# Performance work log

Hardware: AMD Instinct MI355X
Metric: run time of the kernel (lower is better)

## Reference

```python
import jax, jax.numpy as jnp
import numpy as np

INPUT_DIM, HIDDEN_DIM, OUTPUT_DIM = 256, 64, 64
N_NODES, N_EDGES = 100000, 1200000


def setup_inputs() -> dict:
    key = jax.random.key(0)
    k1, k2, k3, k4 = jax.random.split(key, 4)
    x = jax.random.normal(k1, (N_NODES, INPUT_DIM), dtype=jnp.float32)
    edge_index = jax.random.randint(k2, (2, N_EDGES), 0, N_NODES, dtype=jnp.int64)
    # torch Linear weight layout: [out_features, in_features], xavier_uniform init
    def xavier(k, shape):
        fan_out, fan_in = shape
        lim = float(np.sqrt(6.0 / (fan_in + fan_out)))
        return jax.random.uniform(k, shape, minval=-lim, maxval=lim, dtype=jnp.float32)
    W1 = xavier(k3, (HIDDEN_DIM, INPUT_DIM))
    b1 = jnp.zeros((HIDDEN_DIM,), dtype=jnp.float32)
    W2 = xavier(k4, (OUTPUT_DIM, HIDDEN_DIM))
    b2 = jnp.zeros((OUTPUT_DIM,), dtype=jnp.float32)
    return {"x": x, "edge_index": edge_index, "W1": W1, "b1": b1, "W2": W2, "b2": b2}


def reference(x, edge_index, W1, b1, W2, b2):
    N = x.shape[0]
    loops = jnp.arange(N, dtype=edge_index.dtype)
    # GCNConv default: add self-loops, symmetric deg^-1/2 normalization
    src = jnp.concatenate([edge_index[0], loops])  # message sources (x_j)
    dst = jnp.concatenate([edge_index[1], loops])  # aggregation targets
    deg = jax.ops.segment_sum(jnp.ones_like(src, dtype=x.dtype), dst, num_segments=N)
    dinv = jnp.where(deg > 0, jax.lax.rsqrt(jnp.maximum(deg, 1e-12)), 0.0)
    norm = dinv[src] * dinv[dst]  # [E+N]

    def gcn_layer(h, W, b):
        h = h @ W.T                      # dense linear transform [N, out]
        msg = h[src] * norm[:, None]     # gather + scale [E+N, out]
        agg = jax.ops.segment_sum(msg, dst, num_segments=N)  # scatter-add
        return agg + b

    h = jax.nn.relu(gcn_layer(x, W1, b1))
    out = jax.nn.relu(gcn_layer(h, W2, b2))
    return out
```

## Files before the change

### kernel.cpp

```cpp
#include <hip/hip_runtime.h>

static constexpr int NN  = 100000;
static constexpr int NE  = 1200000;
static constexpr int KIN = 256;
static constexpr int HID = 64;

static constexpr int BSH   = 7;
static constexpr int NPB   = 1 << BSH;
static constexpr int NB    = (NN + NPB - 1) / NPB;
static constexpr int CAP   = 4096;
static constexpr int CHUNK = 8192;
static constexpr int NBK   = (NE + CHUNK - 1) / CHUNK;

typedef __attribute__((ext_vector_type(8))) __bf16 bf16v8;
typedef __attribute__((ext_vector_type(4))) float f32x4;

__device__ __forceinline__ float bf2f(unsigned short u) {
  return __uint_as_float(((unsigned int)u) << 16);
}
__device__ __forceinline__ unsigned short f2bf(float f) {
  unsigned int b = __float_as_uint(f);
  return (unsigned short)((b + 0x7FFFu + ((b >> 16) & 1u)) >> 16);
}

__global__ void k_wconv2z(const float* __restrict__ W1, __bf16* __restrict__ Whi1, __bf16* __restrict__ Wlo1,
                          const float* __restrict__ W2, __bf16* __restrict__ Whi2, __bf16* __restrict__ Wlo2,
                          int* __restrict__ gcur) {
  int i = blockIdx.x * 256 + threadIdx.x;
  constexpr int n1 = HID * KIN;
  if (i < n1) {
    float v = W1[i];
    __bf16 h = (__bf16)v;
    Whi1[i] = h;
    Wlo1[i] = (__bf16)(v - (float)h);
  } else if (i < n1 + HID * HID) {
    int j = i - n1;
    float v = W2[j];
    __bf16 h = (__bf16)v;
    Whi2[j] = h;
    Wlo2[j] = (__bf16)(v - (float)h);
  }
  if (i < NB) gcur[i] = 0;
}

__global__ void __launch_bounds__(256) k_bin1p(const int* __restrict__ ed, int* __restrict__ gcur,
                                               unsigned* __restrict__ binned) {
  __shared__ int lcnt[NB];
  __shared__ int lbase[NB];
  int t = threadIdx.x, blk = blockIdx.x;
  for (int i = t; i < NB; i += 256) lcnt[i] = 0;
  __syncthreads();
  int base = blk * CHUNK;
  #pragma unroll
  for (int it = 0; it < CHUNK / 256; ++it) {
    int e = base + it * 256 + t;
    if (e < NE) atomicAdd(&lcnt[ed[NE + e] >> BSH], 1);
  }
  __syncthreads();
  for (int i = t; i < NB; i += 256) {
    int c = lcnt[i];
    lbase[i] = (c > 0) ? atomicAdd(&gcur[i], c) : 0;
    lcnt[i] = 0;
  }
  __syncthreads();
  #pragma unroll
  for (int it = 0; it < CHUNK / 256; ++it) {
    int e = base + it * 256 + t;
    if (e < NE) {
      int src = ed[e];
      int dst = ed[NE + e];
      int b = dst >> BSH;
      int r = atomicAdd(&lcnt[b], 1);
      binned[(size_t)b * CAP + lbase[b] + r] = (unsigned)src | ((unsigned)(dst & (NPB - 1)) << 17);
    }
  }
}

__global__ void __launch_bounds__(256) k_degcsr(const unsigned* __restrict__ binned,
                                                const int* __restrict__ gcur,
                                                int* __restrict__ deg, float* __restrict__ dinv,
                                                int* __restrict__ rp, int* __restrict__ csr) {
  __shared__ int d[NPB];
  __shared__ int sc[NPB];
  __shared__ int cur[NPB];
  int t = threadIdx.x, b = blockIdx.x;
  if (t < NPB) { d[t] = 0; cur[t] = 0; }
  __syncthreads();
  const int n = gcur[b];
  const unsigned* win = binned + (size_t)b * CAP;
  for (int i = t; i < n; i += 256) atomicAdd(&d[win[i] >> 17], 1);
  __syncthreads();
  if (t < NPB) sc[t] = d[t];
  __syncthreads();
  #pragma unroll
  for (int off = 1; off < NPB; off <<= 1) {
    int x = (t < NPB && t >= off) ? sc[t - off] : 0;
    __syncthreads();
    if (t < NPB) sc[t] += x;
    __syncthreads();
  }
  if (t < NPB) {
    int node = b * NPB + t;
    if (node < NN) {
      deg[node] = d[t];
      dinv[node] = rsqrtf((float)(d[t] + 1));
      rp[node] = b * CAP + sc[t] - d[t];
    }
  }
  __syncthreads();
  for (int i = t; i < n; i += 256) {
    unsigned u = win[i];
    int src = (int)(u & 0x1FFFFu);
    int dl  = (int)(u >> 17);
    int r = atomicAdd(&cur[dl], 1);
    csr[(size_t)b * CAP + (sc[dl] - d[dl]) + r] = src;
  }
}

template<int K, int MODE>
__global__ void __launch_bounds__(256, 4)
k_gemm(const float* __restrict__ X, const __bf16* __restrict__ Whi, const __bf16* __restrict__ Wlo,
       const float* __restrict__ dinv, const float* __restrict__ bias, void* __restrict__ Yv) {
  constexpr int KT = 32;
  constexpr int NT = K / KT;
  constexpr int LS = 40;
  constexpr int CS = 68;
  __shared__ __align__(16) char smem[4 * 64 * LS * 2];
  __bf16* xh = (__bf16*)smem;
  __bf16* xl = xh + 64 * LS;
  __bf16* wh = xl + 64 * LS;
  __bf16* wl = wh + 64 * LS;
  float*  cl = (float*)smem;

  const int t = threadIdx.x;
  const int l = t & 63;
  const int wc = (t >> 6) * 16;
  const int rowbase = blockIdx.x * 64;

  f32x4 acc[4];
  #pragma unroll
  for (int rt = 0; rt < 4; ++rt) acc[rt] = (f32x4){0.f, 0.f, 0.f, 0.f};

  const int sr = t >> 2;
  const int kc = (t & 3) * 8;

  for (int kt = 0; kt < NT; ++kt) {
    __syncthreads();
    {
      int gr = rowbase + sr;
      float4 v0 = make_float4(0.f, 0.f, 0.f, 0.f), v1 = v0;
      if (gr < NN) {
        const float* xp = X + (size_t)gr * K + kt * KT + kc;
        v0 = *reinterpret_cast<const float4*>(xp);
        v1 = *reinterpret_cast<const float4*>(xp + 4);
      }
      float e[8] = {v0.x, v0.y, v0.z, v0.w, v1.x, v1.y, v1.z, v1.w};
      bf16v8 hv, lv;
      #pragma unroll
      for (int j = 0; j < 8; ++j) {
        __bf16 h = (__bf16)e[j];
        hv[j] = h;
        lv[j] = (__bf16)(e[j] - (float)h);
      }
      *reinterpret_cast<bf16v8*>(&xh[sr * LS + kc]) = hv;
      *reinterpret_cast<bf16v8*>(&xl[sr * LS + kc]) = lv;
      *reinterpret_cast<bf16v8*>(&wh[sr * LS + kc]) =
          *reinterpret_cast<const bf16v8*>(Whi + (size_t)sr * K + kt * KT + kc);
      *reinterpret_cast<bf16v8*>(&wl[sr * LS + kc]) =
          *reinterpret_cast<const bf16v8*>(Wlo + (size_t)sr * K + kt * KT + kc);
    }
    __syncthreads();

    const int bo = (wc + (l & 15)) * LS + (l >> 4) * 8;
    bf16v8 bh = *reinterpret_cast<const bf16v8*>(&wh[bo]);
    bf16v8 bl = *reinterpret_cast<const bf16v8*>(&wl[bo]);
    #pragma unroll
    for (int rt = 0; rt < 4; ++rt) {
      const int ao = (rt * 16 + (l & 15)) * LS + (l >> 4) * 8;
      bf16v8 ah = *reinterpret_cast<const bf16v8*>(&xh[ao]);
      bf16v8 al = *reinterpret_cast<const bf16v8*>(&xl[ao]);
      acc[rt] = __builtin_amdgcn_mfma_f32_16x16x32_bf16(ah, bh, acc[rt], 0, 0, 0);
      acc[rt] = __builtin_amdgcn_mfma_f32_16x16x32_bf16(al, bh, acc[rt], 0, 0, 0);
      acc[rt] = __builtin_amdgcn_mfma_f32_16x16x32_bf16(ah, bl, acc[rt], 0, 0, 0);
    }
  }

  __syncthreads();
  #pragma unroll
  for (int rt = 0; rt < 4; ++rt)
    #pragma unroll
    for (int j = 0; j < 4; ++j)
      cl[(rt * 16 + (l >> 4) * 4 + j) * CS + wc + (l & 15)] = acc[rt][j];
  __syncthreads();

  const int r = t >> 2, cc = (t & 3) * 16;
  const int grow = rowbase + r;
  if (grow < NN) {
    if (MODE == 0) {
      float dv = dinv[grow];
      bf16v8 o0, o1;
      #pragma unroll
      for (int j = 0; j < 8; ++j) o0[j] = (__bf16)(cl[r * CS + cc + j] * dv);
      #pragma unroll
      for (int j = 0; j < 8; ++j) o1[j] = (__bf16)(cl[r * CS + cc + 8 + j] * dv);
      __bf16* yp = (__bf16*)Yv + (size_t)grow * HID + cc;
      *reinterpret_cast<bf16v8*>(yp) = o0;
      *reinterpret_cast<bf16v8*>(yp + 8) = o1;
    } else {
      float* yp = (float*)Yv + (size_t)grow * HID + cc;
      #pragma unroll
      for (int c4 = 0; c4 < 4; ++c4) {
        float4 o;
        o.x = fmaxf(cl[r * CS + cc + c4 * 4 + 0] + bias[cc + c4 * 4 + 0], 0.f);
        o.y = fmaxf(cl[r * CS + cc + c4 * 4 + 1] + bias[cc + c4 * 4 + 1], 0.f);
        o.z = fmaxf(cl[r * CS + cc + c4 * 4 + 2] + bias[cc + c4 * 4 + 2], 0.f);
        o.w = fmaxf(cl[r * CS + cc + c4 * 4 + 3] + bias[cc + c4 * 4 + 3], 0.f);
        *reinterpret_cast<float4*>(yp + c4 * 4) = o;
      }
    }
  }
}

__global__ void __launch_bounds__(256, 8)
k_agg(const unsigned short* __restrict__ T, const int* __restrict__ csr,
      const int* __restrict__ rp, const int* __restrict__ deg,
      const float* __restrict__ dinv, const float* __restrict__ bias,
      unsigned short* __restrict__ Ov) {
  int node = blockIdx.x * 4 + (threadIdx.x >> 6);
  int lane = threadIdx.x & 63;
  float acc = bf2f(T[(size_t)node * HID + lane]);
  int start = rp[node];
  int len = deg[node];
  for (int base = 0; base < len; base += 64) {
    int m = min(64, len - base);
    int idx = (lane < m) ? csr[start + base + lane] : 0;
    for (int c0 = 0; c0 < m; c0 += 16) {
      float part = 0.f;
      #pragma unroll
      for (int i = 0; i < 16; ++i) {
        int e = c0 + i;
        int s = __shfl(idx, e & 63);
        float v = bf2f(T[(size_t)s * HID + lane]);
        part += (e < m) ? v : 0.f;
      }
      acc += part;
    }
  }
  float dv = dinv[node];
  float h = dv * fmaxf(fmaf(dv, acc, bias[lane]), 0.f);
  Ov[(size_t)node * HID + lane] = f2bf(h);
}

__global__ void __launch_bounds__(256, 8)
k_aggemm(const unsigned short* __restrict__ T, const int* __restrict__ csr,
         const int* __restrict__ rp, const int* __restrict__ deg,
         const float* __restrict__ dinv,
         const __bf16* __restrict__ Whi2, const __bf16* __restrict__ Wlo2,
         const float* __restrict__ bias, float* __restrict__ out) {
  constexpr int LS = 72;
  constexpr int CS = 68;
  __shared__ __align__(16) char smem[2 * 64 * LS * 2];
  __bf16* gh = (__bf16*)smem;
  __bf16* gl = gh + 64 * LS;
  float*  cl = (float*)smem;

  const int t = threadIdx.x;
  const int l = t & 63;
  const int w = t >> 6;
  const int rowbase = blockIdx.x * 64;

  for (int i = 0; i < 16; ++i) {
    int node = rowbase + w * 16 + i;
    float gv = 0.f;
    if (node < NN) {
      float acc = bf2f(T[(size_t)node * HID + l]);
      int start = rp[node];
      int len = deg[node];
      for (int base = 0; base < len; base += 64) {
        int m = min(64, len - base);
        int idx = (l < m) ? csr[start + base + l] : 0;
        for (int c0 = 0; c0 < m; c0 += 16) {
          float part = 0.f;
          #pragma unroll
          for (int j = 0; j < 16; ++j) {
            int e = c0 + j;
            int s = __shfl(idx, e & 63);
            float v = bf2f(T[(size_t)s * HID + l]);
            part += (e < m) ? v : 0.f;
          }
          acc += part;
        }
      }
      gv = dinv[node] * acc;
    }
    __bf16 h = (__bf16)gv;
    int r = w * 16 + i;
    gh[r * LS + l] = h;
    gl[r * LS + l] = (__bf16)(gv - (float)h);
  }
  __syncthreads();

  const int wc = w * 16;
  f32x4 acc[4];
  #pragma unroll
  for (int rt = 0; rt < 4; ++rt) acc[rt] = (f32x4){0.f, 0.f, 0.f, 0.f};
  #pragma unroll
  for (int kc = 0; kc < 2; ++kc) {
    const size_t wo = (size_t)(wc + (l & 15)) * HID + kc * 32 + (l >> 4) * 8;
    bf16v8 bh = *reinterpret_cast<const bf16v8*>(Whi2 + wo);
    bf16v8 bl = *reinterpret_cast<const bf16v8*>(Wlo2 + wo);
    #pragma unroll
    for (int rt = 0; rt < 4; ++rt) {
      const int ao = (rt * 16 + (l & 15)) * LS + kc * 32 + (l >> 4) * 8;
      bf16v8 ah = *reinterpret_cast<const bf16v8*>(&gh[ao]);
      bf16v8 al = *reinterpret_cast<const bf16v8*>(&gl[ao]);
      acc[rt] = __builtin_amdgcn_mfma_f32_16x16x32_bf16(ah, bh, acc[rt], 0, 0, 0);
      acc[rt] = __builtin_amdgcn_mfma_f32_16x16x32_bf16(al, bh, acc[rt], 0, 0, 0);
      acc[rt] = __builtin_amdgcn_mfma_f32_16x16x32_bf16(ah, bl, acc[rt], 0, 0, 0);
    }
  }
  __syncthreads();
  #pragma unroll
  for (int rt = 0; rt < 4; ++rt)
    #pragma unroll
    for (int j = 0; j < 4; ++j)
      cl[(rt * 16 + (l >> 4) * 4 + j) * CS + wc + (l & 15)] = acc[rt][j];
  __syncthreads();

  const int r = t >> 2, cc = (t & 3) * 16;
  const int grow = rowbase + r;
  if (grow < NN) {
    float* yp = out + (size_t)grow * HID + cc;
    #pragma unroll
    for (int c4 = 0; c4 < 4; ++c4) {
      float4 o;
      o.x = fmaxf(cl[r * CS + cc + c4 * 4 + 0] + bias[cc + c4 * 4 + 0], 0.f);
      o.y = fmaxf(cl[r * CS + cc + c4 * 4 + 1] + bias[cc + c4 * 4 + 1], 0.f);
      o.z = fmaxf(cl[r * CS + cc + c4 * 4 + 2] + bias[cc + c4 * 4 + 2], 0.f);
      o.w = fmaxf(cl[r * CS + cc + c4 * 4 + 3] + bias[cc + c4 * 4 + 3], 0.f);
      *reinterpret_cast<float4*>(yp + c4 * 4) = o;
    }
  }
}

extern "C" void kernel_launch(void* const* d_in, const int* in_sizes, int n_in,
                              void* d_out, int out_size, void* d_ws, size_t ws_size,
                              hipStream_t stream) {
  const float* x  = (const float*)d_in[0];
  const int*   ed = (const int*)d_in[1];
  const float* W1 = (const float*)d_in[2];
  const float* b1 = (const float*)d_in[3];
  const float* W2 = (const float*)d_in[4];
  const float* b2 = (const float*)d_in[5];
  float* out = (float*)d_out;

  char* ws = (char*)d_ws;
  size_t off = 0;
  auto alloc = [&](size_t bytes) {
    char* p = ws + off;
    off = (off + bytes + 255) & ~(size_t)255;
    return p;
  };
  int*      deg    = (int*)alloc((size_t)NN * 4);
  float*    dinv   = (float*)alloc((size_t)NN * 4);
  int*      rp     = (int*)alloc((size_t)NN * 4);
  int*      gcur   = (int*)alloc((size_t)NB * 4);
  unsigned* binned = (unsigned*)alloc((size_t)NB * CAP * 4);
  int*      csr    = (int*)alloc((size_t)NB * CAP * 4);
  unsigned short* T1 = (unsigned short*)alloc((size_t)NN * HID * 2);
  unsigned short* Hp = (unsigned short*)alloc((size_t)NN * HID * 2);
  __bf16*   Whi1   = (__bf16*)alloc((size_t)HID * KIN * 2);
  __bf16*   Wlo1   = (__bf16*)alloc((size_t)HID * KIN * 2);
  __bf16*   Whi2   = (__bf16*)alloc((size_t)HID * HID * 2);
  __bf16*   Wlo2   = (__bf16*)alloc((size_t)HID * HID * 2);

  k_wconv2z<<<(HID * KIN + HID * HID + 255) / 256, 256, 0, stream>>>(W1, Whi1, Wlo1, W2, Whi2, Wlo2, gcur);
  k_bin1p<<<NBK, 256, 0, stream>>>(ed, gcur, binned);
  k_degcsr<<<NB, 256, 0, stream>>>(binned, gcur, deg, dinv, rp, csr);

  const int GB = (NN + 63) / 64;

  k_gemm<KIN, 0><<<GB, 256, 0, stream>>>(x, Whi1, Wlo1, dinv, b1, (void*)T1);
  k_agg<<<NN / 4, 256, 0, stream>>>(T1, csr, rp, deg, dinv, b1, Hp);

  k_aggemm<<<GB, 256, 0, stream>>>(Hp, csr, rp, deg, dinv, Whi2, Wlo2, b2, out);
}
```

Baseline: 154.3 us.

## Prefetch GEMM tiles into registers and interleave two-node gathers in aggregation

The first-layer GEMM now loads the next K tile from global memory into registers while the MFMAs for the current tile run, then writes it to shared memory behind a barrier. This hides global load latency at the cost of extra registers and an extra barrier per iteration. Both aggregation kernels now make each wavefront process two nodes at once, issuing both nodes' 16 gathered loads before reducing them. This raises memory-level parallelism, and launch bounds are lowered from 8 to 6 to leave room for the extra registers, which risks lower occupancy and divergence when the two nodes have different degrees.

Result: slower. 157.9 us (+2.4%).

```diff
diff --git a/kernel.cpp b/kernel.cpp
--- a/kernel.cpp
+++ b/kernel.cpp
@@ -143,33 +143,44 @@
 
   const int sr = t >> 2;
   const int kc = (t & 3) * 8;
+  const int gr = rowbase + sr;
+  const float* xrow = X + (size_t)gr * K + kc;
+
+  float4 pa, pb;
+  bf16v8 pwh, pwl;
+
+  auto loadTile = [&](int kt) {
+    pa = make_float4(0.f, 0.f, 0.f, 0.f);
+    pb = pa;
+    if (gr < NN) {
+      pa = *reinterpret_cast<const float4*>(xrow + kt * KT);
+      pb = *reinterpret_cast<const float4*>(xrow + kt * KT + 4);
+    }
+    size_t wo = (size_t)sr * K + kt * KT + kc;
+    pwh = *reinterpret_cast<const bf16v8*>(Whi + wo);
+    pwl = *reinterpret_cast<const bf16v8*>(Wlo + wo);
+  };
+  auto storeTile = [&]() {
+    float e[8] = {pa.x, pa.y, pa.z, pa.w, pb.x, pb.y, pb.z, pb.w};
+    bf16v8 hv, lv;
+    #pragma unroll
+    for (int j = 0; j < 8; ++j) {
+      __bf16 h = (__bf16)e[j];
+      hv[j] = h;
+      lv[j] = (__bf16)(e[j] - (float)h);
+    }
+    *reinterpret_cast<bf16v8*>(&xh[sr * LS + kc]) = hv;
+    *reinterpret_cast<bf16v8*>(&xl[sr * LS + kc]) = lv;
+    *reinterpret_cast<bf16v8*>(&wh[sr * LS + kc]) = pwh;
+    *reinterpret_cast<bf16v8*>(&wl[sr * LS + kc]) = pwl;
+  };
+
+  loadTile(0);
+  storeTile();
+  __syncthreads();
 
   for (int kt = 0; kt < NT; ++kt) {
-    __syncthreads();
-    {
-      int gr = rowbase + sr;
-      float4 v0 = make_float4(0.f, 0.f, 0.f, 0.f), v1 = v0;
-      if (gr < NN) {
-        const float* xp = X + (size_t)gr * K + kt * KT + kc;
-        v0 = *reinterpret_cast<const float4*>(xp);
-        v1 = *reinterpret_cast<const float4*>(xp + 4);
-      }
-      float e[8] = {v0.x, v0.y, v0.z, v0.w, v1.x, v1.y, v1.z, v1.w};
-      bf16v8 hv, lv;
-      #pragma unroll
-      for (int j = 0; j < 8; ++j) {
-        __bf16 h = (__bf16)e[j];
-        hv[j] = h;
-        lv[j] = (__bf16)(e[j] - (float)h);
-      }
-      *reinterpret_cast<bf16v8*>(&xh[sr * LS + kc]) = hv;
-      *reinterpret_cast<bf16v8*>(&xl[sr * LS + kc]) = lv;
-      *reinterpret_cast<bf16v8*>(&wh[sr * LS + kc]) =
-          *reinterpret_cast<const bf16v8*>(Whi + (size_t)sr * K + kt * KT + kc);
-      *reinterpret_cast<bf16v8*>(&wl[sr * LS + kc]) =
-          *reinterpret_cast<const bf16v8*>(Wlo + (size_t)sr * K + kt * KT + kc);
-    }
-    __syncthreads();
+    if (kt + 1 < NT) loadTile(kt + 1);
 
     const int bo = (wc + (l & 15)) * LS + (l >> 4) * 8;
     bf16v8 bh = *reinterpret_cast<const bf16v8*>(&wh[bo]);
@@ -182,6 +193,12 @@
       acc[rt] = __builtin_amdgcn_mfma_f32_16x16x32_bf16(ah, bh, acc[rt], 0, 0, 0);
       acc[rt] = __builtin_amdgcn_mfma_f32_16x16x32_bf16(al, bh, acc[rt], 0, 0, 0);
       acc[rt] = __builtin_amdgcn_mfma_f32_16x16x32_bf16(ah, bl, acc[rt], 0, 0, 0);
+    }
+
+    if (kt + 1 < NT) {
+      __syncthreads();
+      storeTile();
+      __syncthreads();
     }
   }
 
@@ -221,37 +238,63 @@
   }
 }
 
-__global__ void __launch_bounds__(256, 8)
+__global__ void __launch_bounds__(256, 6)
 k_agg(const unsigned short* __restrict__ T, const int* __restrict__ csr,
       const int* __restrict__ rp, const int* __restrict__ deg,
       const float* __restrict__ dinv, const float* __restrict__ bias,
       unsigned short* __restrict__ Ov) {
-  int node = blockIdx.x * 4 + (threadIdx.x >> 6);
-  int lane = threadIdx.x & 63;
-  float acc = bf2f(T[(size_t)node * HID + lane]);
-  int start = rp[node];
-  int len = deg[node];
-  for (int base = 0; base < len; base += 64) {
-    int m = min(64, len - base);
-    int idx = (lane < m) ? csr[start + base + lane] : 0;
-    for (int c0 = 0; c0 < m; c0 += 16) {
-      float part = 0.f;
-      #pragma unroll
-      for (int i = 0; i < 16; ++i) {
-        int e = c0 + i;
-        int s = __shfl(idx, e & 63);
-        float v = bf2f(T[(size_t)s * HID + lane]);
-        part += (e < m) ? v : 0.f;
-      }
-      acc += part;
-    }
-  }
-  float dv = dinv[node];
-  float h = dv * fmaxf(fmaf(dv, acc, bias[lane]), 0.f);
-  Ov[(size_t)node * HID + lane] = f2bf(h);
-}
-
-__global__ void __launch_bounds__(256, 8)
+  const int lane = threadIdx.x & 63;
+  const int n0 = blockIdx.x * 8 + (threadIdx.x >> 6) * 2;
+  const int n1 = n0 + 1;
+  float acc0 = bf2f(T[(size_t)n0 * HID + lane]);
+  float acc1 = bf2f(T[(size_t)n1 * HID + lane]);
+  const int s0 = rp[n0], l0 = deg[n0];
+  const int s1 = rp[n1], l1 = deg[n1];
+  const int lmax = max(l0, l1);
+  for (int base = 0; base < lmax; base += 64) {
+    const int m0 = min(64, l0 - base);
+    const int m1 = min(64, l1 - base);
+    int idx0 = (lane < m0) ? csr[s0 + base + lane] : 0;
+    int idx1 = (lane < m1) ? csr[s1 + base + lane] : 0;
+    const int cmax = max(m0, m1);
+    for (int c0 = 0; c0 < cmax; c0 += 16) {
+      float v0[16], v1[16];
+      const bool a0 = c0 < m0, a1 = c0 < m1;
+      if (a0) {
+        #pragma unroll
+        for (int i = 0; i < 16; ++i) {
+          int s = __shfl(idx0, (c0 + i) & 63);
+          v0[i] = bf2f(T[(size_t)s * HID + lane]);
+        }
+      }
+      if (a1) {
+        #pragma unroll
+        for (int i = 0; i < 16; ++i) {
+          int s = __shfl(idx1, (c0 + i) & 63);
+          v1[i] = bf2f(T[(size_t)s * HID + lane]);
+        }
+      }
+      if (a0) {
+        float p = 0.f;
+        #pragma unroll
+        for (int i = 0; i < 16; ++i) p += (c0 + i < m0) ? v0[i] : 0.f;
+        acc0 += p;
+      }
+      if (a1) {
+        float p = 0.f;
+        #pragma unroll
+        for (int i = 0; i < 16; ++i) p += (c0 + i < m1) ? v1[i] : 0.f;
+        acc1 += p;
+      }
+    }
+  }
+  float dv0 = dinv[n0];
+  Ov[(size_t)n0 * HID + lane] = f2bf(dv0 * fmaxf(fmaf(dv0, acc0, bias[lane]), 0.f));
+  float dv1 = dinv[n1];
+  Ov[(size_t)n1 * HID + lane] = f2bf(dv1 * fmaxf(fmaf(dv1, acc1, bias[lane]), 0.f));
+}
+
+__global__ void __launch_bounds__(256, 6)
 k_aggemm(const unsigned short* __restrict__ T, const int* __restrict__ csr,
          const int* __restrict__ rp, const int* __restrict__ deg,
          const float* __restrict__ dinv,
@@ -269,34 +312,60 @@
   const int w = t >> 6;
   const int rowbase = blockIdx.x * 64;
 
-  for (int i = 0; i < 16; ++i) {
-    int node = rowbase + w * 16 + i;
-    float gv = 0.f;
-    if (node < NN) {
-      float acc = bf2f(T[(size_t)node * HID + l]);
-      int start = rp[node];
-      int len = deg[node];
-      for (int base = 0; base < len; base += 64) {
-        int m = min(64, len - base);
-        int idx = (l < m) ? csr[start + base + l] : 0;
-        for (int c0 = 0; c0 < m; c0 += 16) {
-          float part = 0.f;
+  for (int i = 0; i < 16; i += 2) {
+    const int n0 = rowbase + w * 16 + i;
+    const int n1 = n0 + 1;
+    const bool va0 = n0 < NN, va1 = n1 < NN;
+    float acc0 = va0 ? bf2f(T[(size_t)n0 * HID + l]) : 0.f;
+    float acc1 = va1 ? bf2f(T[(size_t)n1 * HID + l]) : 0.f;
+    const int s0 = va0 ? rp[n0] : 0, l0 = va0 ? deg[n0] : 0;
+    const int s1 = va1 ? rp[n1] : 0, l1 = va1 ? deg[n1] : 0;
+    const int lmax = max(l0, l1);
+    for (int base = 0; base < lmax; base += 64) {
+      const int m0 = min(64, l0 - base);
+      const int m1 = min(64, l1 - base);
+      int idx0 = (l < m0) ? csr[s0 + base + l] : 0;
+      int idx1 = (l < m1) ? csr[s1 + base + l] : 0;
+      const int cmax = max(m0, m1);
+      for (int c0 = 0; c0 < cmax; c0 += 16) {
+        float v0[16], v1[16];
+        const bool a0 = c0 < m0, a1 = c0 < m1;
+        if (a0) {
           #pragma unroll
           for (int j = 0; j < 16; ++j) {
-            int e = c0 + j;
-            int s = __shfl(idx, e & 63);
-            float v = bf2f(T[(size_t)s * HID + l]);
-            part += (e < m) ? v : 0.f;
+            int s = __shfl(idx0, (c0 + j) & 63);
+            v0[j] = bf2f(T[(size_t)s * HID + l]);
           }
-          acc += part;
-        }
-      }
-      gv = dinv[node] * acc;
-    }
-    __bf16 h = (__bf16)gv;
-    int r = w * 16 + i;
-    gh[r * LS + l] = h;
-    gl[r * LS + l] = (__bf16)(gv - (float)h);
+        }
+        if (a1) {
+          #pragma unroll
+          for (int j = 0; j < 16; ++j) {
+            int s = __shfl(idx1, (c0 + j) & 63);
+            v1[j] = bf2f(T[(size_t)s * HID + l]);
+          }
+        }
+        if (a0) {
+          float p = 0.f;
+          #pragma unroll
+          for (int j = 0; j < 16; ++j) p += (c0 + j < m0) ? v0[j] : 0.f;
+          acc0 += p;
+        }
+        if (a1) {
+          float p = 0.f;
+          #pragma unroll
+          for (int j = 0; j < 16; ++j) p += (c0 + j < m1) ? v1[j] : 0.f;
+          acc1 += p;
+        }
+      }
+    }
+    float g0 = va0 ? dinv[n0] * acc0 : 0.f;
+    float g1 = va1 ? dinv[n1] * acc1 : 0.f;
+    __bf16 h0 = (__bf16)g0, h1 = (__bf16)g1;
+    const int r0 = w * 16 + i;
+    gh[r0 * LS + l] = h0;
+    gl[r0 * LS + l] = (__bf16)(g0 - (float)h0);
+    gh[(r0 + 1) * LS + l] = h1;
+    gl[(r0 + 1) * LS + l] = (__bf16)(g1 - (float)h1);
   }
   __syncthreads();
 
@@ -381,7 +450,7 @@
   const int GB = (NN + 63) / 64;
 
   k_gemm<KIN, 0><<<GB, 256, 0, stream>>>(x, Whi1, Wlo1, dinv, b1, (void*)T1);
-  k_agg<<<NN / 4, 256, 0, stream>>>(T1, csr, rp, deg, dinv, b1, Hp);
+  k_agg<<<NN / 8, 256, 0, stream>>>(T1, csr, rp, deg, dinv, b1, Hp);
 
   k_aggemm<<<GB, 256, 0, stream>>>(Hp, csr, rp, deg, dinv, Whi2, Wlo2, b2, out);
 }
```

## Prefetch GEMM tiles into registers and gather two bf16 features per lane

Applied to the files above, without the earlier changes.

The first-layer GEMM now loads the next K tile from global memory into registers while MFMAs run on the current shared-memory tile, overlapping load latency with compute. Both aggregation kernels now read packed 32-bit words holding two bf16 features. Each half-wave handles alternate edges, so every gather instruction covers two neighbour rows, and the two halves are combined with a lane shuffle. This is meant to cut gather instruction count and raise bytes per load, at the cost of more registers. k_aggemm's launch bounds are lowered from 8 to 6 to allow for that.

After: 145.5 us. 5.7% less time.

```diff
diff --git a/kernel.cpp b/kernel.cpp
--- a/kernel.cpp
+++ b/kernel.cpp
@@ -143,33 +143,44 @@
 
   const int sr = t >> 2;
   const int kc = (t & 3) * 8;
+  const int gr = rowbase + sr;
+  const float* xrow = X + (size_t)gr * K + kc;
+
+  float4 pa, pb;
+  bf16v8 pwh, pwl;
+
+  auto loadTile = [&](int kt) {
+    pa = make_float4(0.f, 0.f, 0.f, 0.f);
+    pb = pa;
+    if (gr < NN) {
+      pa = *reinterpret_cast<const float4*>(xrow + kt * KT);
+      pb = *reinterpret_cast<const float4*>(xrow + kt * KT + 4);
+    }
+    size_t wo = (size_t)sr * K + kt * KT + kc;
+    pwh = *reinterpret_cast<const bf16v8*>(Whi + wo);
+    pwl = *reinterpret_cast<const bf16v8*>(Wlo + wo);
+  };
+  auto storeTile = [&]() {
+    float e[8] = {pa.x, pa.y, pa.z, pa.w, pb.x, pb.y, pb.z, pb.w};
+    bf16v8 hv, lv;
+    #pragma unroll
+    for (int j = 0; j < 8; ++j) {
+      __bf16 h = (__bf16)e[j];
+      hv[j] = h;
+      lv[j] = (__bf16)(e[j] - (float)h);
+    }
+    *reinterpret_cast<bf16v8*>(&xh[sr * LS + kc]) = hv;
+    *reinterpret_cast<bf16v8*>(&xl[sr * LS + kc]) = lv;
+    *reinterpret_cast<bf16v8*>(&wh[sr * LS + kc]) = pwh;
+    *reinterpret_cast<bf16v8*>(&wl[sr * LS + kc]) = pwl;
+  };
+
+  loadTile(0);
+  storeTile();
+  __syncthreads();
 
   for (int kt = 0; kt < NT; ++kt) {
-    __syncthreads();
-    {
-      int gr = rowbase + sr;
-      float4 v0 = make_float4(0.f, 0.f, 0.f, 0.f), v1 = v0;
-      if (gr < NN) {
-        const float* xp = X + (size_t)gr * K + kt * KT + kc;
-        v0 = *reinterpret_cast<const float4*>(xp);
-        v1 = *reinterpret_cast<const float4*>(xp + 4);
-      }
-      float e[8] = {v0.x, v0.y, v0.z, v0.w, v1.x, v1.y, v1.z, v1.w};
-      bf16v8 hv, lv;
-      #pragma unroll
-      for (int j = 0; j < 8; ++j) {
-        __bf16 h = (__bf16)e[j];
-        hv[j] = h;
-        lv[j] = (__bf16)(e[j] - (float)h);
-      }
-      *reinterpret_cast<bf16v8*>(&xh[sr * LS + kc]) = hv;
-      *reinterpret_cast<bf16v8*>(&xl[sr * LS + kc]) = lv;
-      *reinterpret_cast<bf16v8*>(&wh[sr * LS + kc]) =
-          *reinterpret_cast<const bf16v8*>(Whi + (size_t)sr * K + kt * KT + kc);
-      *reinterpret_cast<bf16v8*>(&wl[sr * LS + kc]) =
-          *reinterpret_cast<const bf16v8*>(Wlo + (size_t)sr * K + kt * KT + kc);
-    }
-    __syncthreads();
+    if (kt + 1 < NT) loadTile(kt + 1);
 
     const int bo = (wc + (l & 15)) * LS + (l >> 4) * 8;
     bf16v8 bh = *reinterpret_cast<const bf16v8*>(&wh[bo]);
@@ -182,6 +193,12 @@
       acc[rt] = __builtin_amdgcn_mfma_f32_16x16x32_bf16(ah, bh, acc[rt], 0, 0, 0);
       acc[rt] = __builtin_amdgcn_mfma_f32_16x16x32_bf16(al, bh, acc[rt], 0, 0, 0);
       acc[rt] = __builtin_amdgcn_mfma_f32_16x16x32_bf16(ah, bl, acc[rt], 0, 0, 0);
+    }
+
+    if (kt + 1 < NT) {
+      __syncthreads();
+      storeTile();
+      __syncthreads();
     }
   }
 
@@ -222,37 +239,52 @@
 }
 
 __global__ void __launch_bounds__(256, 8)
-k_agg(const unsigned short* __restrict__ T, const int* __restrict__ csr,
+k_agg(const unsigned* __restrict__ T32, const int* __restrict__ csr,
       const int* __restrict__ rp, const int* __restrict__ deg,
       const float* __restrict__ dinv, const float* __restrict__ bias,
-      unsigned short* __restrict__ Ov) {
-  int node = blockIdx.x * 4 + (threadIdx.x >> 6);
-  int lane = threadIdx.x & 63;
-  float acc = bf2f(T[(size_t)node * HID + lane]);
-  int start = rp[node];
-  int len = deg[node];
+      unsigned* __restrict__ Ov32) {
+  const int t = threadIdx.x;
+  const int node = blockIdx.x * 4 + (t >> 6);
+  const int lane = t & 63;
+  const int s = lane >> 5;
+  const int fp = lane & 31;
+  float acc0 = 0.f, acc1 = 0.f;
+  const int start = rp[node];
+  const int len = deg[node];
   for (int base = 0; base < len; base += 64) {
     int m = min(64, len - base);
     int idx = (lane < m) ? csr[start + base + lane] : 0;
     for (int c0 = 0; c0 < m; c0 += 16) {
-      float part = 0.f;
+      float p0 = 0.f, p1 = 0.f;
       #pragma unroll
-      for (int i = 0; i < 16; ++i) {
-        int e = c0 + i;
-        int s = __shfl(idx, e & 63);
-        float v = bf2f(T[(size_t)s * HID + lane]);
-        part += (e < m) ? v : 0.f;
+      for (int i = 0; i < 8; ++i) {
+        int e = c0 + 2 * i + s;
+        int src = __shfl(idx, e & 63);
+        unsigned u = T32[(size_t)src * 32 + fp];
+        bool ok = e < m;
+        p0 += ok ? __uint_as_float(u << 16) : 0.f;
+        p1 += ok ? __uint_as_float(u & 0xFFFF0000u) : 0.f;
       }
-      acc += part;
-    }
-  }
+      acc0 += p0;
+      acc1 += p1;
+    }
+  }
+  acc0 += __shfl_xor(acc0, 32);
+  acc1 += __shfl_xor(acc1, 32);
+  unsigned su = T32[(size_t)node * 32 + fp];
+  acc0 += __uint_as_float(su << 16);
+  acc1 += __uint_as_float(su & 0xFFFF0000u);
   float dv = dinv[node];
-  float h = dv * fmaxf(fmaf(dv, acc, bias[lane]), 0.f);
-  Ov[(size_t)node * HID + lane] = f2bf(h);
-}
-
-__global__ void __launch_bounds__(256, 8)
-k_aggemm(const unsigned short* __restrict__ T, const int* __restrict__ csr,
+  float h0 = dv * fmaxf(fmaf(dv, acc0, bias[fp * 2]), 0.f);
+  float h1 = dv * fmaxf(fmaf(dv, acc1, bias[fp * 2 + 1]), 0.f);
+  if (s == 0) {
+    unsigned pack = (unsigned)f2bf(h0) | ((unsigned)f2bf(h1) << 16);
+    Ov32[(size_t)node * 32 + fp] = pack;
+  }
+}
+
+__global__ void __launch_bounds__(256, 6)
+k_aggemm(const unsigned* __restrict__ T32, const int* __restrict__ csr,
          const int* __restrict__ rp, const int* __restrict__ deg,
          const float* __restrict__ dinv,
          const __bf16* __restrict__ Whi2, const __bf16* __restrict__ Wlo2,
@@ -267,36 +299,59 @@
   const int t = threadIdx.x;
   const int l = t & 63;
   const int w = t >> 6;
+  const int s = l >> 5;
+  const int fp = l & 31;
   const int rowbase = blockIdx.x * 64;
 
   for (int i = 0; i < 16; ++i) {
-    int node = rowbase + w * 16 + i;
-    float gv = 0.f;
-    if (node < NN) {
-      float acc = bf2f(T[(size_t)node * HID + l]);
-      int start = rp[node];
-      int len = deg[node];
-      for (int base = 0; base < len; base += 64) {
-        int m = min(64, len - base);
-        int idx = (l < m) ? csr[start + base + l] : 0;
-        for (int c0 = 0; c0 < m; c0 += 16) {
-          float part = 0.f;
-          #pragma unroll
-          for (int j = 0; j < 16; ++j) {
-            int e = c0 + j;
-            int s = __shfl(idx, e & 63);
-            float v = bf2f(T[(size_t)s * HID + l]);
-            part += (e < m) ? v : 0.f;
-          }
-          acc += part;
+    const int node = rowbase + w * 16 + i;
+    const bool va = node < NN;
+    float acc0 = 0.f, acc1 = 0.f;
+    const int start = va ? rp[node] : 0;
+    const int len = va ? deg[node] : 0;
+    for (int base = 0; base < len; base += 64) {
+      int m = min(64, len - base);
+      int idx = (l < m) ? csr[start + base + l] : 0;
+      for (int c0 = 0; c0 < m; c0 += 16) {
+        float p0 = 0.f, p1 = 0.f;
+        #pragma unroll
+        for (int j = 0; j < 8; ++j) {
+          int e = c0 + 2 * j + s;
+          int src = __shfl(idx, e & 63);
+          unsigned u = T32[(size_t)src * 32 + fp];
+          bool ok = e < m;
+          p0 += ok ? __uint_as_float(u << 16) : 0.f;
+          p1 += ok ? __uint_as_float(u & 0xFFFF0000u) : 0.f;
         }
+        acc0 += p0;
+        acc1 += p1;
       }
-      gv = dinv[node] * acc;
-    }
-    __bf16 h = (__bf16)gv;
-    int r = w * 16 + i;
-    gh[r * LS + l] = h;
-    gl[r * LS + l] = (__bf16)(gv - (float)h);
+    }
+    acc0 += __shfl_xor(acc0, 32);
+    acc1 += __shfl_xor(acc1, 32);
+    float g0 = 0.f, g1 = 0.f;
+    if (va) {
+      unsigned su = T32[(size_t)node * 32 + fp];
+      acc0 += __uint_as_float(su << 16);
+      acc1 += __uint_as_float(su & 0xFFFF0000u);
+      float dv = dinv[node];
+      g0 = dv * acc0;
+      g1 = dv * acc1;
+    }
+    __bf16 h0 = (__bf16)g0, h1 = (__bf16)g1;
+    __bf16 lo0 = (__bf16)(g0 - (float)h0), lo1 = (__bf16)(g1 - (float)h1);
+    if (s == 0) {
+      const int r = w * 16 + i;
+      unsigned hp, lp;
+      {
+        unsigned short a = *(unsigned short*)&h0, b = *(unsigned short*)&h1;
+        hp = (unsigned)a | ((unsigned)b << 16);
+        unsigned short c = *(unsigned short*)&lo0, d = *(unsigned short*)&lo1;
+        lp = (unsigned)c | ((unsigned)d << 16);
+      }
+      *reinterpret_cast<unsigned*>(&gh[r * LS + fp * 2]) = hp;
+      *reinterpret_cast<unsigned*>(&gl[r * LS + fp * 2]) = lp;
+    }
   }
   __syncthreads();
 
@@ -367,8 +422,8 @@
   int*      gcur   = (int*)alloc((size_t)NB * 4);
   unsigned* binned = (unsigned*)alloc((size_t)NB * CAP * 4);
   int*      csr    = (int*)alloc((size_t)NB * CAP * 4);
-  unsigned short* T1 = (unsigned short*)alloc((size_t)NN * HID * 2);
-  unsigned short* Hp = (unsigned short*)alloc((size_t)NN * HID * 2);
+  unsigned* T1     = (unsigned*)alloc((size_t)NN * HID * 2);
+  unsigned* Hp     = (unsigned*)alloc((size_t)NN * HID * 2);
   __bf16*   Whi1   = (__bf16*)alloc((size_t)HID * KIN * 2);
   __bf16*   Wlo1   = (__bf16*)alloc((size_t)HID * KIN * 2);
   __bf16*   Whi2   = (__bf16*)alloc((size_t)HID * HID * 2);
```
